# Performance work log

Hardware: AMD Instinct MI355X
Metric: run time of the kernel (lower is better)

## Reference

```python
import jax, jax.numpy as jnp
import numpy as np

N, E, C, D, H = 50000, 1600000, 50000, 128, 512


def setup_inputs() -> dict:
    key = jax.random.key(0)
    ks = jax.random.split(key, 16)
    s = jnp.float32(0.02)  # keep activations stable through 3 layers
    inp = {}
    inp["x"] = jax.random.normal(ks[0], (N, D), jnp.float32)
    inp["edge_index"] = jax.random.randint(ks[1], (2, E), 0, N)
    inp["first_edge"] = jax.random.randint(ks[2], (2,), 0, N)
    inp["candidate_edges"] = jax.random.randint(ks[3], (C, 2), 0, N)
    inp["t"] = jax.random.uniform(ks[4], (1, 1), jnp.float32)
    dims = [(D, H), (H, H), (H, H)]
    i = 5
    for l, (di, do) in enumerate(dims):
        inp[f"gin{l}_w1"] = jax.random.normal(ks[i], (di, do), jnp.float32) * s; i += 1
        inp[f"gin{l}_b1"] = jnp.zeros((do,), jnp.float32)
        inp[f"gin{l}_w2"] = jax.random.normal(ks[i], (do, do), jnp.float32) * s; i += 1
        inp[f"gin{l}_b2"] = jnp.zeros((do,), jnp.float32)
    inp["pred_w1"] = jax.random.normal(ks[i], (5 * H, H), jnp.float32) * s; i += 1
    inp["pred_b1"] = jnp.zeros((H,), jnp.float32)
    inp["pred_w2"] = jax.random.normal(ks[i], (H, 1), jnp.float32) * s; i += 1
    inp["pred_b2"] = jnp.zeros((1,), jnp.float32)
    inp["time_w1"] = jax.random.normal(ks[i], (1, H), jnp.float32) * s; i += 1
    inp["time_b1"] = jnp.zeros((H,), jnp.float32)
    inp["time_w2"] = jax.random.normal(ks[i], (H, H), jnp.float32) * s; i += 1
    inp["time_b2"] = jnp.zeros((H,), jnp.float32)
    return inp


def _edge_rep(x, u, v):
    # 'sum_absdiff': cat([x_u + x_v, |x_u - x_v|]) -> 2*H features
    xu, xv = x[u], x[v]
    return jnp.concatenate([xu + xv, jnp.abs(xu - xv)], axis=-1)


def reference(x, edge_index, first_edge, candidate_edges, t,
              gin0_w1, gin0_b1, gin0_w2, gin0_b2,
              gin1_w1, gin1_b1, gin1_w2, gin1_b2,
              gin2_w1, gin2_b1, gin2_w2, gin2_b2,
              pred_w1, pred_b1, pred_w2, pred_b2,
              time_w1, time_b1, time_w2, time_b2):
    src, dst = edge_index[0], edge_index[1]
    layers = [(gin0_w1, gin0_b1, gin0_w2, gin0_b2),
              (gin1_w1, gin1_b1, gin1_w2, gin1_b2),
              (gin2_w1, gin2_b1, gin2_w2, gin2_b2)]
    # GINConv (eps=0): h_i = MLP(x_i + sum_{j->i} x_j)
    for w1, b1, w2, b2 in layers:
        agg = jax.ops.segment_sum(x[src], dst, num_segments=x.shape[0])
        h = x + agg
        x = jax.nn.relu(h @ w1 + b1) @ w2 + b2
    first_feat = _edge_rep(x, first_edge[0], first_edge[1])  # [2H]
    t_embed = (jax.nn.relu(t @ time_w1 + time_b1) @ time_w2 + time_b2)[0]  # [H]
    cand_feat = _edge_rep(x, candidate_edges[:, 0], candidate_edges[:, 1])  # [C, 2H]
    Cn = cand_feat.shape[0]
    feat = jnp.concatenate([
        jnp.broadcast_to(first_feat, (Cn, first_feat.shape[0])),
        cand_feat,
        jnp.broadcast_to(t_embed, (Cn, t_embed.shape[0])),
    ], axis=-1)  # [C, 5H]
    logits = (jax.nn.relu(feat @ pred_w1 + pred_b1) @ pred_w2 + pred_b2)[:, 0]  # [C]
    return logits
```

## Files before the change

kernel.cpp:

```cpp
#include <hip/hip_runtime.h>

typedef __bf16 bf16x2 __attribute__((ext_vector_type(2)));
typedef __bf16 bf16x4 __attribute__((ext_vector_type(4)));
typedef __bf16 bf16x8 __attribute__((ext_vector_type(8)));
typedef float f32x4 __attribute__((ext_vector_type(4)));

#define CSR_CHUNKS 256

__device__ __forceinline__ void gload16(const __bf16* g, __bf16* l) {
    __builtin_amdgcn_global_load_lds((const __attribute__((address_space(1))) void*)g,
                                     (__attribute__((address_space(3))) void*)l, 16, 0, 0);
}

__global__ __launch_bounds__(256)
void hist_part_kernel(const int* __restrict__ dst, int* __restrict__ deg, int E, int N) {
    const int r = blockIdx.x & 7;
    const int chunk = blockIdx.x >> 3;
    const int RS = (N + 7) >> 3;
    const int lo = r * RS;
    const int hi = min(lo + RS, N);
    const int stride = CSR_CHUNKS * 256;
    for (int i = chunk * 256 + threadIdx.x; i < E; i += stride) {
        int d = dst[i];
        if (d >= lo && d < hi) atomicAdd(&deg[d], 1);
    }
}

__global__ __launch_bounds__(256)
void scatter_part_kernel(const int* __restrict__ src, const int* __restrict__ dst,
                         int* __restrict__ cursor, int* __restrict__ colsrc, int E, int N) {
    const int r = blockIdx.x & 7;
    const int chunk = blockIdx.x >> 3;
    const int RS = (N + 7) >> 3;
    const int lo = r * RS;
    const int hi = min(lo + RS, N);
    const int stride = CSR_CHUNKS * 256;
    for (int i = chunk * 256 + threadIdx.x; i < E; i += stride) {
        int d = dst[i];
        if (d >= lo && d < hi) {
            int p = atomicAdd(&cursor[d], 1);
            colsrc[p] = src[i];
        }
    }
}

__global__ __launch_bounds__(256)
void blocksum_kernel(const int* __restrict__ deg, int* __restrict__ bsum, int n) {
    __shared__ int red[256];
    int i = blockIdx.x * 256 + threadIdx.x;
    red[threadIdx.x] = (i < n) ? deg[i] : 0;
    __syncthreads();
    for (int off = 128; off > 0; off >>= 1) {
        if (threadIdx.x < off) red[threadIdx.x] += red[threadIdx.x + off];
        __syncthreads();
    }
    if (threadIdx.x == 0) bsum[blockIdx.x] = red[0];
}

__global__ __launch_bounds__(256)
void scanb_kernel(int* __restrict__ bsum, int nb) {
    __shared__ int s[256];
    int t = threadIdx.x;
    s[t] = (t < nb) ? bsum[t] : 0;
    __syncthreads();
    for (int off = 1; off < 256; off <<= 1) {
        int v = (t >= off) ? s[t - off] : 0;
        __syncthreads();
        s[t] += v;
        __syncthreads();
    }
    if (t < nb) bsum[t] = (t == 0) ? 0 : s[t - 1];
}

__global__ __launch_bounds__(256)
void scanw_kernel(const int* __restrict__ deg, const int* __restrict__ bsum,
                  int* __restrict__ rowptr, int* __restrict__ cursor, int n) {
    __shared__ int s[256];
    int b = blockIdx.x, t = threadIdx.x;
    int i = b * 256 + t;
    int d = (i < n) ? deg[i] : 0;
    s[t] = d;
    __syncthreads();
    for (int off = 1; off < 256; off <<= 1) {
        int v = (t >= off) ? s[t - off] : 0;
        __syncthreads();
        s[t] += v;
        __syncthreads();
    }
    int incl = s[t];
    int base = bsum[b];
    if (i < n) {
        int r = base + incl - d;
        rowptr[i] = r;
        cursor[i] = r;
        if (i == n - 1) rowptr[n] = base + incl;
    }
}

__global__ void f32_to_bf16_kernel(const float* __restrict__ in, __bf16* __restrict__ out, int n4) {
    int i = blockIdx.x * 256 + threadIdx.x;
    if (i < n4) {
        float4 f = ((const float4*)in)[i];
        bf16x4 o;
        o[0] = (__bf16)f.x; o[1] = (__bf16)f.y; o[2] = (__bf16)f.z; o[3] = (__bf16)f.w;
        ((bf16x4*)out)[i] = o;
    }
}

__global__ void wprep_kernel(const float* __restrict__ in, __bf16* __restrict__ out, int kbits) {
    int idx = blockIdx.x * 256 + threadIdx.x;
    int K = 1 << kbits;
    if (idx < (512 << kbits)) {
        int k = idx & (K - 1);
        int n = idx >> kbits;
        out[idx] = (__bf16)in[k * 512 + n];
    }
}

template<int F> struct VecT;
template<> struct VecT<2> { using T = bf16x2; };
template<> struct VecT<4> { using T = bf16x4; };
template<> struct VecT<8> { using T = bf16x8; };

template<int F, int U, int STR>
__global__ __launch_bounds__(256)
void agg_kernel(const __bf16* __restrict__ xb, const int* __restrict__ rowptr,
                const int* __restrict__ colsrc, __bf16* __restrict__ h, int n, int colbase) {
    const int node = blockIdx.x * 4 + (threadIdx.x >> 6);
    if (node >= n) return;
    const int lane = threadIdx.x & 63;
    using V = typename VecT<F>::T;

    const __bf16* xl = xb + colbase + lane * F;

    float acc[F];
    {
        V v = *(const V*)(xl + (size_t)node * STR);
        #pragma unroll
        for (int i = 0; i < F; i++) acc[i] = (float)v[i];
    }

    int e   = __builtin_amdgcn_readfirstlane(rowptr[node]);
    int end = __builtin_amdgcn_readfirstlane(rowptr[node + 1]);

    for (; e + U <= end; e += U) {
        int s[U];
        #pragma unroll
        for (int j = 0; j < U; j++) s[j] = colsrc[e + j];
        V v[U];
        #pragma unroll
        for (int j = 0; j < U; j++) v[j] = *(const V*)(xl + (size_t)s[j] * STR);
        #pragma unroll
        for (int j = 0; j < U; j++)
            #pragma unroll
            for (int i = 0; i < F; i++) acc[i] += (float)v[j][i];
    }
    if constexpr (U > 4) {
        for (; e + 4 <= end; e += 4) {
            int s[4];
            #pragma unroll
            for (int j = 0; j < 4; j++) s[j] = colsrc[e + j];
            V v[4];
            #pragma unroll
            for (int j = 0; j < 4; j++) v[j] = *(const V*)(xl + (size_t)s[j] * STR);
            #pragma unroll
            for (int j = 0; j < 4; j++)
                #pragma unroll
                for (int i = 0; i < F; i++) acc[i] += (float)v[j][i];
        }
    }
    for (; e < end; e++) {
        int s0 = colsrc[e];
        V v = *(const V*)(xl + (size_t)s0 * STR);
        #pragma unroll
        for (int i = 0; i < F; i++) acc[i] += (float)v[i];
    }

    __bf16* out = h + colbase + (size_t)node * STR + lane * F;
    V o;
    #pragma unroll
    for (int i = 0; i < F; i++) o[i] = (__bf16)acc[i];
    *(V*)out = o;
}

template<int AMODE, bool RELU>
__global__ __launch_bounds__(256, 3)
void gemm_kernel(const __bf16* __restrict__ A, const __bf16* __restrict__ Xb,
                 const int* __restrict__ cand, const __bf16* __restrict__ Bt,
                 const float* __restrict__ bias, __bf16* __restrict__ Cout,
                 int M, int K) {
    __shared__ __bf16 smem[2 * (2048 + 8192)];
    __bf16* const sA0 = smem;
    __bf16* const sA1 = smem + 2048;
    __bf16* const sB0 = smem + 4096;
    __bf16* const sB1 = smem + 4096 + 8192;

    const int tid = threadIdx.x;
    const int lane = tid & 63;
    const int wid = tid >> 6;
    const int mlane = lane & 15;
    const int quad = lane >> 4;
    const int rowBase = blockIdx.x * 64;
    const int nBase = blockIdx.y * 256;

    const int swzc = (((lane & 3) ^ ((lane >> 3) & 3)) << 3);

    const int aRow = rowBase + wid * 16 + (lane >> 2);
    const __bf16* aSrc = A + (size_t)aRow * K + swzc;
    const int bRow = nBase + wid * 64 + (lane >> 2);
    const __bf16* bSrc = Bt + (size_t)bRow * K + swzc;

    const int rkey = (mlane >> 1) & 3;
    const int base_r = mlane * 32 + ((quad ^ rkey) << 3);

    const int ar = tid >> 2;
    const int acn = tid & 3;
    const int ac = acn << 3;
    const int wkey = (ar >> 1) & 3;
    const int woffA = ar * 32 + ((acn ^ wkey) << 3);

    const f32x4 fzero = {0.f, 0.f, 0.f, 0.f};
    f32x4 acc[4][4];
    #pragma unroll
    for (int i = 0; i < 4; i++)
        #pragma unroll
        for (int j = 0; j < 4; j++) acc[i][j] = fzero;

    int uu = 0, vv = 0;
    const int grow = rowBase + ar;
    const bool arowok = (grow < M);
    if (AMODE == 1 && arowok) { uu = cand[2 * grow]; vv = cand[2 * grow + 1]; }

    bf16x8 pxu{}, pxv{};
    int pk = 0;

    auto stageB = [&](__bf16* bufB, int k0) {
        #pragma unroll
        for (int j = 0; j < 4; j++)
            gload16(bSrc + (size_t)j * 16 * K + k0, bufB + wid * 2048 + j * 512);
    };
    auto stageA0 = [&](__bf16* bufA, int k0) {
        if (aRow < M) gload16(aSrc + k0, bufA + wid * 512);
    };
    auto issueA1 = [&](int k0) {
        pk = k0;
        if (arowok) {
            int kk = (k0 + ac) & 511;
            pxu = *(const bf16x8*)(Xb + (size_t)uu * 512 + kk);
            pxv = *(const bf16x8*)(Xb + (size_t)vv * 512 + kk);
        }
    };
    auto commitA1 = [&](__bf16* bufA) {
        bf16x8 av = bf16x8{};
        if (arowok) {
            if (pk + ac < 512) {
                #pragma unroll
                for (int q = 0; q < 8; q++) av[q] = (__bf16)((float)pxu[q] + (float)pxv[q]);
            } else {
                #pragma unroll
                for (int q = 0; q < 8; q++) av[q] = (__bf16)fabsf((float)pxu[q] - (float)pxv[q]);
            }
        }
        *(bf16x8*)(bufA + woffA) = av;
    };

    auto compute = [&](const __bf16* bufA, const __bf16* bufB) {
        bf16x8 aF[4], bF[4];
        #pragma unroll
        for (int mt = 0; mt < 4; mt++)
            aF[mt] = *(const bf16x8*)(bufA + mt * 512 + base_r);
        #pragma unroll
        for (int nt = 0; nt < 4; nt++)
            bF[nt] = *(const bf16x8*)(bufB + wid * 2048 + nt * 512 + base_r);
        #pragma unroll
        for (int mt = 0; mt < 4; mt++)
            #pragma unroll
            for (int nt = 0; nt < 4; nt++)
                acc[mt][nt] = __builtin_amdgcn_mfma_f32_16x16x32_bf16(aF[mt], bF[nt], acc[mt][nt], 0, 0, 0);
    };

    const int nt = K >> 5;
    if (AMODE == 0) {
        stageA0(sA0, 0);
        stageB(sB0, 0);
        __syncthreads();
        for (int t = 0; t < nt; t += 2) {
            stageA0(sA1, (t + 1) << 5);
            stageB(sB1, (t + 1) << 5);
            compute(sA0, sB0);
            __syncthreads();
            if (t + 2 < nt) {
                stageA0(sA0, (t + 2) << 5);
                stageB(sB0, (t + 2) << 5);
            }
            compute(sA1, sB1);
            __syncthreads();
        }
    } else {
        issueA1(0);
        commitA1(sA0);
        stageB(sB0, 0);
        __syncthreads();
        for (int t = 0; t < nt; t += 2) {
            issueA1((t + 1) << 5);
            stageB(sB1, (t + 1) << 5);
            compute(sA0, sB0);
            commitA1(sA1);
            __syncthreads();
            if (t + 2 < nt) {
                issueA1((t + 2) << 5);
                stageB(sB0, (t + 2) << 5);
            }
            compute(sA1, sB1);
            if (t + 2 < nt) commitA1(sA0);
            __syncthreads();
        }
    }

    float bv[4];
    #pragma unroll
    for (int nt2 = 0; nt2 < 4; nt2++) bv[nt2] = bias[nBase + wid * 64 + nt2 * 16 + mlane];

    float* tp = (float*)smem;
    const int erow = tid >> 4;
    const int ecg = tid & 15;
    #pragma unroll
    for (int mt = 0; mt < 4; mt++) {
        __syncthreads();
        #pragma unroll
        for (int nt2 = 0; nt2 < 4; nt2++) {
            #pragma unroll
            for (int r = 0; r < 4; r++) {
                float v = acc[mt][nt2][r] + bv[nt2];
                if (RELU) v = fmaxf(v, 0.f);
                tp[(quad * 4 + r) * 260 + wid * 64 + nt2 * 16 + mlane] = v;
            }
        }
        __syncthreads();
        int gr = rowBase + mt * 16 + erow;
        if (gr < M) {
            const float* rp = tp + erow * 260 + ecg * 16;
            f32x4 a = *(const f32x4*)(rp);
            f32x4 b = *(const f32x4*)(rp + 4);
            f32x4 c = *(const f32x4*)(rp + 8);
            f32x4 d = *(const f32x4*)(rp + 12);
            bf16x8 o0, o1;
            #pragma unroll
            for (int j = 0; j < 4; j++) { o0[j] = (__bf16)a[j]; o0[4 + j] = (__bf16)b[j]; }
            #pragma unroll
            for (int j = 0; j < 4; j++) { o1[j] = (__bf16)c[j]; o1[4 + j] = (__bf16)d[j]; }
            __bf16* op = Cout + (size_t)gr * 512 + nBase + ecg * 16;
            *(bf16x8*)op = o0;
            *(bf16x8*)(op + 8) = o1;
        }
    }
}

__global__ __launch_bounds__(512)
void constvec_kernel(const __bf16* __restrict__ xb, const int* __restrict__ first_edge,
                     const float* __restrict__ t,
                     const float* __restrict__ tw1, const float* __restrict__ tb1,
                     const float* __restrict__ tw2, const float* __restrict__ tb2,
                     const float* __restrict__ pw1, const float* __restrict__ pb1,
                     float* __restrict__ cvec) {
    __shared__ float z1[512];
    __shared__ float te[512];
    __shared__ float ff[1024];
    int tid = threadIdx.x;
    float tv = t[0];
    z1[tid] = fmaxf(tv * tw1[tid] + tb1[tid], 0.f);
    int u = first_edge[0], v = first_edge[1];
    float xu = (float)xb[(size_t)u * 512 + tid];
    float xv = (float)xb[(size_t)v * 512 + tid];
    ff[tid] = xu + xv;
    ff[512 + tid] = fabsf(xu - xv);
    __syncthreads();
    float s = tb2[tid];
    for (int j = 0; j < 512; j++) s += z1[j] * tw2[j * 512 + tid];
    te[tid] = s;
    __syncthreads();
    float c = pb1[tid];
    for (int k = 0; k < 1024; k++) c += ff[k] * pw1[k * 512 + tid];
    for (int j = 0; j < 512; j++) c += te[j] * pw1[(2048 + j) * 512 + tid];
    cvec[tid] = c;
}

__global__ __launch_bounds__(256)
void logits_kernel(const __bf16* __restrict__ Z, const float* __restrict__ w2,
                   const float* __restrict__ b2, float* __restrict__ out, int C) {
    int c = blockIdx.x * 4 + (threadIdx.x >> 6);
    if (c >= C) return;
    int lane = threadIdx.x & 63;
    bf16x8 z = *(const bf16x8*)(Z + (size_t)c * 512 + lane * 8);
    const float4* w = (const float4*)(w2 + lane * 8);
    float4 w0 = w[0], w1 = w[1];
    float s = (float)z[0] * w0.x + (float)z[1] * w0.y + (float)z[2] * w0.z + (float)z[3] * w0.w
            + (float)z[4] * w1.x + (float)z[5] * w1.y + (float)z[6] * w1.z + (float)z[7] * w1.w;
    #pragma unroll
    for (int off = 32; off > 0; off >>= 1) s += __shfl_down(s, off);
    if (lane == 0) out[c] = s + b2[0];
}

extern "C" void kernel_launch(void* const* d_in, const int* in_sizes, int n_in,
                              void* d_out, int out_size, void* d_ws, size_t ws_size,
                              hipStream_t stream) {
    (void)n_in; (void)out_size; (void)ws_size;
    const float* x          = (const float*)d_in[0];
    const int*   edge_index = (const int*)d_in[1];
    const int*   first_edge = (const int*)d_in[2];
    const int*   cand       = (const int*)d_in[3];
    const float* t          = (const float*)d_in[4];
    const float* gw1[3] = {(const float*)d_in[5], (const float*)d_in[9],  (const float*)d_in[13]};
    const float* gb1[3] = {(const float*)d_in[6], (const float*)d_in[10], (const float*)d_in[14]};
    const float* gw2[3] = {(const float*)d_in[7], (const float*)d_in[11], (const float*)d_in[15]};
    const float* gb2[3] = {(const float*)d_in[8], (const float*)d_in[12], (const float*)d_in[16]};
    const float* pw1 = (const float*)d_in[17];
    const float* pb1 = (const float*)d_in[18];
    const float* pw2 = (const float*)d_in[19];
    const float* pb2 = (const float*)d_in[20];
    const float* tw1 = (const float*)d_in[21];
    const float* tb1 = (const float*)d_in[22];
    const float* tw2 = (const float*)d_in[23];
    const float* tb2 = (const float*)d_in[24];

    const int N = in_sizes[0] / 128;
    const int E = in_sizes[1] / 2;
    const int C = in_sizes[3] / 2;

    char* p = (char*)d_ws;
    auto alloc = [&](size_t bytes) -> void* {
        void* r = (void*)p;
        p += (bytes + 255) & ~(size_t)255;
        return r;
    };
    __bf16* h    = (__bf16*)alloc((size_t)N * 512 * 2);
    __bf16* u    = (__bf16*)alloc((size_t)N * 512 * 2);
    __bf16* xb   = (__bf16*)alloc((size_t)N * 512 * 2);
    __bf16* wt01 = (__bf16*)alloc((size_t)512 * 128 * 2);
    __bf16* wt02 = (__bf16*)alloc((size_t)512 * 512 * 2);
    __bf16* wt11 = (__bf16*)alloc((size_t)512 * 512 * 2);
    __bf16* wt12 = (__bf16*)alloc((size_t)512 * 512 * 2);
    __bf16* wt21 = (__bf16*)alloc((size_t)512 * 512 * 2);
    __bf16* wt22 = (__bf16*)alloc((size_t)512 * 512 * 2);
    __bf16* wtH  = (__bf16*)alloc((size_t)512 * 1024 * 2);
    int* rowptr = (int*)alloc((size_t)(N + 1) * 4);
    int* deg    = (int*)alloc((size_t)N * 4);
    int* cursor = (int*)alloc((size_t)N * 4);
    int* colsrc = (int*)alloc((size_t)E * 4);
    int* bsum   = (int*)alloc((size_t)256 * 4);
    float* cvec = (float*)alloc(512 * 4);
    __bf16* xb0 = (__bf16*)u;

    const int* src = edge_index;
    const int* dst = edge_index + E;

    hipMemsetAsync(deg, 0, (size_t)N * 4, stream);
    int nb = (N + 255) / 256;
    hist_part_kernel<<<CSR_CHUNKS * 8, 256, 0, stream>>>(dst, deg, E, N);
    blocksum_kernel<<<nb, 256, 0, stream>>>(deg, bsum, N);
    scanb_kernel<<<1, 256, 0, stream>>>(bsum, nb);
    scanw_kernel<<<nb, 256, 0, stream>>>(deg, bsum, rowptr, cursor, N);
    scatter_part_kernel<<<CSR_CHUNKS * 8, 256, 0, stream>>>(src, dst, cursor, colsrc, E, N);

    f32_to_bf16_kernel<<<((N * 128 / 4) + 255) / 256, 256, 0, stream>>>(x, xb0, N * 128 / 4);
    wprep_kernel<<<((512 << 7)  + 255) / 256, 256, 0, stream>>>(gw1[0], wt01, 7);
    wprep_kernel<<<((512 << 9)  + 255) / 256, 256, 0, stream>>>(gw2[0], wt02, 9);
    wprep_kernel<<<((512 << 9)  + 255) / 256, 256, 0, stream>>>(gw1[1], wt11, 9);
    wprep_kernel<<<((512 << 9)  + 255) / 256, 256, 0, stream>>>(gw2[1], wt12, 9);
    wprep_kernel<<<((512 << 9)  + 255) / 256, 256, 0, stream>>>(gw1[2], wt21, 9);
    wprep_kernel<<<((512 << 9)  + 255) / 256, 256, 0, stream>>>(gw2[2], wt22, 9);
    wprep_kernel<<<((512 << 10) + 255) / 256, 256, 0, stream>>>(pw1 + (size_t)1024 * 512, wtH, 10);

    dim3 ggrid((N + 63) / 64, 2);
    int ablocks = (N + 3) / 4;

    agg_kernel<2, 16, 128><<<ablocks, 256, 0, stream>>>(xb0, rowptr, colsrc, h, N, 0);
    gemm_kernel<0, true ><<<ggrid, 256, 0, stream>>>(h, nullptr, nullptr, wt01, gb1[0], u,  N, 128);
    gemm_kernel<0, false><<<ggrid, 256, 0, stream>>>(u, nullptr, nullptr, wt02, gb2[0], xb, N, 512);
    agg_kernel<4, 8, 512><<<ablocks, 256, 0, stream>>>(xb, rowptr, colsrc, h, N, 0);
    agg_kernel<4, 8, 512><<<ablocks, 256, 0, stream>>>(xb, rowptr, colsrc, h, N, 256);
    gemm_kernel<0, true ><<<ggrid, 256, 0, stream>>>(h, nullptr, nullptr, wt11, gb1[1], u,  N, 512);
    gemm_kernel<0, false><<<ggrid, 256, 0, stream>>>(u, nullptr, nullptr, wt12, gb2[1], xb, N, 512);
    agg_kernel<4, 8, 512><<<ablocks, 256, 0, stream>>>(xb, rowptr, colsrc, h, N, 0);
    agg_kernel<4, 8, 512><<<ablocks, 256, 0, stream>>>(xb, rowptr, colsrc, h, N, 256);
    gemm_kernel<0, true ><<<ggrid, 256, 0, stream>>>(h, nullptr, nullptr, wt21, gb1[2], u,  N, 512);
    gemm_kernel<0, false><<<ggrid, 256, 0, stream>>>(u, nullptr, nullptr, wt22, gb2[2], xb, N, 512);

    constvec_kernel<<<1, 512, 0, stream>>>(xb, first_edge, t, tw1, tb1, tw2, tb2, pw1, pb1, cvec);
    dim3 hgrid((C + 63) / 64, 2);
    gemm_kernel<1, true><<<hgrid, 256, 0, stream>>>(nullptr, xb, cand, wtH, cvec, u, C, 1024);
    logits_kernel<<<(C + 3) / 4, 256, 0, stream>>>(u, pw2, pb2, (float*)d_out, C);
}
```

Before: 1.202 ms.

## Keep two tile loads in flight with explicit vmcnt waits in GEMM loop

Restructures the AMODE==0 GEMM main loop so the next k-tile's global-to-LDS loads stay in flight while the current tile computes. Explicit s_waitcnt vmcnt(5) partial waits, raw s_barrier and sched_barrier calls replace the full __syncthreads drains. Out-of-range A rows are clamped to row M-1 so every thread issues a fixed number of loads, which keeps the vmcnt counting exact. The cost is reliance on precise counter accounting, and clamped rows load duplicate data that must not be stored.

```diff
diff --git a/kernel.cpp b/kernel.cpp
--- a/kernel.cpp
+++ b/kernel.cpp
@@ -206,7 +206,8 @@
     const int swzc = (((lane & 3) ^ ((lane >> 3) & 3)) << 3);
 
     const int aRow = rowBase + wid * 16 + (lane >> 2);
-    const __bf16* aSrc = A + (size_t)aRow * K + swzc;
+    const int aRowC = (aRow < M) ? aRow : (M - 1);
+    const __bf16* aSrc = A + (size_t)aRowC * K + swzc;
     const int bRow = nBase + wid * 64 + (lane >> 2);
     const __bf16* bSrc = Bt + (size_t)bRow * K + swzc;
 
@@ -240,7 +241,7 @@
             gload16(bSrc + (size_t)j * 16 * K + k0, bufB + wid * 2048 + j * 512);
     };
     auto stageA0 = [&](__bf16* bufA, int k0) {
-        if (aRow < M) gload16(aSrc + k0, bufA + wid * 512);
+        gload16(aSrc + k0, bufA + wid * 512);
     };
     auto issueA1 = [&](int k0) {
         pk = k0;
@@ -283,18 +284,32 @@
     if (AMODE == 0) {
         stageA0(sA0, 0);
         stageB(sB0, 0);
-        __syncthreads();
-        for (int t = 0; t < nt; t += 2) {
-            stageA0(sA1, (t + 1) << 5);
-            stageB(sB1, (t + 1) << 5);
-            compute(sA0, sB0);
-            __syncthreads();
-            if (t + 2 < nt) {
-                stageA0(sA0, (t + 2) << 5);
-                stageB(sB0, (t + 2) << 5);
+        __builtin_amdgcn_sched_barrier(0);
+        stageA0(sA1, 32);
+        stageB(sB1, 32);
+        asm volatile("s_waitcnt vmcnt(5)" ::: "memory");
+        __builtin_amdgcn_s_barrier();
+        __builtin_amdgcn_sched_barrier(0);
+
+        int cur = 0;
+        for (int t = 0; t < nt; ++t) {
+            __bf16* cA = cur ? sA1 : sA0;
+            __bf16* cB = cur ? sB1 : sB0;
+            compute(cA, cB);
+            if (t + 1 < nt) {
+                __builtin_amdgcn_s_barrier();
+                __builtin_amdgcn_sched_barrier(0);
+                if (t + 2 < nt) {
+                    stageA0(cA, (t + 2) << 5);
+                    stageB(cB, (t + 2) << 5);
+                    asm volatile("s_waitcnt vmcnt(5)" ::: "memory");
+                } else {
+                    asm volatile("s_waitcnt vmcnt(0)" ::: "memory");
+                }
+                __builtin_amdgcn_s_barrier();
+                __builtin_amdgcn_sched_barrier(0);
+                cur ^= 1;
             }
-            compute(sA1, sB1);
-            __syncthreads();
         }
     } else {
         issueA1(0);
```

Measured after the change: 1.201 ms. No clear change (-0.1%).

## Add 8-wave 128x256-tile GEMM with interleaved load/MFMA schedule for GIN layers

Applied to the files above, without the earlier changes.

Adds a new 512-thread GEMM kernel that computes a 128x256 output tile per block, with waves arranged 2x4 and a K-step of 64 split into four phases. Each phase interleaves LDS fragment reads, async global-to-LDS prefetch of the next tile, explicit barriers, waitcnts and setprio around MFMA bursts. It replaces the 256-thread 64x256 GEMM for all six GIN MLP matmuls, and the old kernel keeps only its candidate-gather mode. The aim is more data reuse per block and better overlap of memory with compute. In exchange it runs one block per CU with large LDS use, and clamping out-of-range A rows to M-1 means redundant loads on the tail tile.

```diff
diff --git a/kernel.cpp b/kernel.cpp
--- a/kernel.cpp
+++ b/kernel.cpp
@@ -183,6 +183,177 @@
     *(V*)out = o;
 }
 
+#define LDv(p) (*(const bf16x8*)(p))
+#define MM8(NTP) \
+  { acc[0][2*(NTP)]   = __builtin_amdgcn_mfma_f32_16x16x32_bf16(aF[0], bF0, acc[0][2*(NTP)],   0,0,0); \
+    acc[1][2*(NTP)]   = __builtin_amdgcn_mfma_f32_16x16x32_bf16(aF[1], bF0, acc[1][2*(NTP)],   0,0,0); \
+    acc[2][2*(NTP)]   = __builtin_amdgcn_mfma_f32_16x16x32_bf16(aF[2], bF0, acc[2][2*(NTP)],   0,0,0); \
+    acc[3][2*(NTP)]   = __builtin_amdgcn_mfma_f32_16x16x32_bf16(aF[3], bF0, acc[3][2*(NTP)],   0,0,0); \
+    acc[0][2*(NTP)+1] = __builtin_amdgcn_mfma_f32_16x16x32_bf16(aF[0], bF1, acc[0][2*(NTP)+1], 0,0,0); \
+    acc[1][2*(NTP)+1] = __builtin_amdgcn_mfma_f32_16x16x32_bf16(aF[1], bF1, acc[1][2*(NTP)+1], 0,0,0); \
+    acc[2][2*(NTP)+1] = __builtin_amdgcn_mfma_f32_16x16x32_bf16(aF[2], bF1, acc[2][2*(NTP)+1], 0,0,0); \
+    acc[3][2*(NTP)+1] = __builtin_amdgcn_mfma_f32_16x16x32_bf16(aF[3], bF1, acc[3][2*(NTP)+1], 0,0,0); }
+
+template<bool RELU>
+__global__ __launch_bounds__(512, 1)
+void gemm8_kernel(const __bf16* __restrict__ A, const __bf16* __restrict__ Bt,
+                  const float* __restrict__ bias, __bf16* __restrict__ Cout,
+                  int M, int K) {
+    __shared__ __bf16 smem[49152];
+    __bf16* const sA0 = smem;
+    __bf16* const sA1 = smem + 8192;
+    __bf16* const sB0 = smem + 16384;
+    __bf16* const sB1 = smem + 32768;
+
+    const int tid = threadIdx.x;
+    const int lane = tid & 63;
+    const int w = tid >> 6;
+    const int wr = w >> 2;
+    const int wc = w & 3;
+    const int mlane = lane & 15;
+    const int quad = lane >> 4;
+    const int rowBase = blockIdx.x * 128;
+    const int nBase = blockIdx.y * 256;
+
+    const int swz = (((lane & 3) ^ ((lane >> 3) & 3)) << 3);
+    int aR = rowBase + w * 16 + (lane >> 2);
+    if (aR >= M) aR = M - 1;
+    const __bf16* aSrc = A + (size_t)aR * K + swz;
+    const int bR0 = nBase + w * 16 + (lane >> 2);
+    const __bf16* bSrc = Bt + (size_t)bR0 * K + swz;
+
+    const int rkey = (mlane >> 1) & 3;
+    const int aRdBase = wr * 2048 + mlane * 32 + ((quad ^ rkey) << 3);
+    const int bRdBase = wc * 2048 + mlane * 32 + ((quad ^ rkey) << 3);
+
+    f32x4 acc[4][4];
+    #pragma unroll
+    for (int i = 0; i < 4; i++)
+        #pragma unroll
+        for (int j = 0; j < 4; j++) acc[i][j] = f32x4{0.f, 0.f, 0.f, 0.f};
+
+    auto stA = [&](__bf16* nbuf, int k0, int kk) {
+        gload16(aSrc + k0 + kk * 32, nbuf + kk * 4096 + w * 512);
+    };
+    auto stB = [&](__bf16* nbuf, int k0, int kk, int h) {
+        gload16(bSrc + (size_t)(h * 128) * K + k0 + kk * 32,
+                nbuf + kk * 8192 + h * 4096 + w * 512);
+    };
+
+    bf16x8 aF[4], bF0, bF1;
+
+    stA(sA0, 0, 0); stB(sB0, 0, 0, 0); stB(sB0, 0, 0, 1);
+    stA(sA0, 0, 1); stB(sB0, 0, 1, 0); stB(sB0, 0, 1, 1);
+    asm volatile("s_waitcnt vmcnt(3)" ::: "memory");
+    __builtin_amdgcn_sched_barrier(0);
+    __builtin_amdgcn_s_barrier();
+
+    const int NT = K >> 6;
+    for (int t = 0; t < NT; ++t) {
+        __bf16* const cA = (t & 1) ? sA1 : sA0;
+        __bf16* const cB = (t & 1) ? sB1 : sB0;
+        __bf16* const nA = (t & 1) ? sA0 : sA1;
+        __bf16* const nB = (t & 1) ? sB0 : sB1;
+        const int kn = (t + 1) << 6;
+        const bool more = (t + 1 < NT);
+
+        aF[0] = LDv(cA + aRdBase);
+        aF[1] = LDv(cA + 512 + aRdBase);
+        aF[2] = LDv(cA + 1024 + aRdBase);
+        aF[3] = LDv(cA + 1536 + aRdBase);
+        bF0 = LDv(cB + bRdBase);
+        bF1 = LDv(cB + 512 + bRdBase);
+        if (more) { stA(nA, kn, 0); stB(nB, kn, 0, 0); }
+        __builtin_amdgcn_s_barrier();
+        asm volatile("s_waitcnt lgkmcnt(0)" ::: "memory");
+        __builtin_amdgcn_sched_barrier(0);
+        __builtin_amdgcn_s_setprio(1);
+        MM8(0);
+        __builtin_amdgcn_s_setprio(0);
+        __builtin_amdgcn_s_barrier();
+
+        bF0 = LDv(cB + 1024 + bRdBase);
+        bF1 = LDv(cB + 1536 + bRdBase);
+        if (more) stB(nB, kn, 0, 1);
+        __builtin_amdgcn_s_barrier();
+        asm volatile("s_waitcnt lgkmcnt(0)" ::: "memory");
+        __builtin_amdgcn_sched_barrier(0);
+        __builtin_amdgcn_s_setprio(1);
+        MM8(1);
+        __builtin_amdgcn_s_setprio(0);
+        if (more) { asm volatile("s_waitcnt vmcnt(3)" ::: "memory"); }
+        else      { asm volatile("s_waitcnt vmcnt(0)" ::: "memory"); }
+        __builtin_amdgcn_sched_barrier(0);
+        __builtin_amdgcn_s_barrier();
+
+        aF[0] = LDv(cA + 4096 + aRdBase);
+        aF[1] = LDv(cA + 4096 + 512 + aRdBase);
+        aF[2] = LDv(cA + 4096 + 1024 + aRdBase);
+        aF[3] = LDv(cA + 4096 + 1536 + aRdBase);
+        bF0 = LDv(cB + 8192 + bRdBase);
+        bF1 = LDv(cB + 8192 + 512 + bRdBase);
+        if (more) { stA(nA, kn, 1); stB(nB, kn, 1, 0); }
+        __builtin_amdgcn_s_barrier();
+        asm volatile("s_waitcnt lgkmcnt(0)" ::: "memory");
+        __builtin_amdgcn_sched_barrier(0);
+        __builtin_amdgcn_s_setprio(1);
+        MM8(0);
+        __builtin_amdgcn_s_setprio(0);
+        __builtin_amdgcn_s_barrier();
+
+        bF0 = LDv(cB + 8192 + 1024 + bRdBase);
+        bF1 = LDv(cB + 8192 + 1536 + bRdBase);
+        if (more) stB(nB, kn, 1, 1);
+        __builtin_amdgcn_s_barrier();
+        asm volatile("s_waitcnt lgkmcnt(0)" ::: "memory");
+        __builtin_amdgcn_sched_barrier(0);
+        __builtin_amdgcn_s_setprio(1);
+        MM8(1);
+        __builtin_amdgcn_s_setprio(0);
+        if (more) { asm volatile("s_waitcnt vmcnt(3)" ::: "memory"); }
+        __builtin_amdgcn_sched_barrier(0);
+        __builtin_amdgcn_s_barrier();
+    }
+
+    float bv[4];
+    #pragma unroll
+    for (int nt = 0; nt < 4; nt++) bv[nt] = bias[nBase + wc * 64 + nt * 16 + mlane];
+
+    float* tp = (float*)smem;
+    const int srow = tid >> 4;
+    const int scg = tid & 15;
+    #pragma unroll
+    for (int mt = 0; mt < 4; mt++) {
+        __syncthreads();
+        #pragma unroll
+        for (int nt = 0; nt < 4; nt++) {
+            #pragma unroll
+            for (int r = 0; r < 4; r++) {
+                float v = acc[mt][nt][r] + bv[nt];
+                if (RELU) v = fmaxf(v, 0.f);
+                tp[(wr * 16 + quad * 4 + r) * 260 + wc * 64 + nt * 16 + mlane] = v;
+            }
+        }
+        __syncthreads();
+        int gr = rowBase + (srow >> 4) * 64 + mt * 16 + (srow & 15);
+        if (gr < M) {
+            const float* rp = tp + srow * 260 + scg * 16;
+            f32x4 a = *(const f32x4*)(rp);
+            f32x4 b = *(const f32x4*)(rp + 4);
+            f32x4 c = *(const f32x4*)(rp + 8);
+            f32x4 d = *(const f32x4*)(rp + 12);
+            bf16x8 o0, o1;
+            #pragma unroll
+            for (int j = 0; j < 4; j++) { o0[j] = (__bf16)a[j]; o0[4 + j] = (__bf16)b[j]; }
+            #pragma unroll
+            for (int j = 0; j < 4; j++) { o1[j] = (__bf16)c[j]; o1[4 + j] = (__bf16)d[j]; }
+            __bf16* op = Cout + (size_t)gr * 512 + nBase + scg * 16;
+            *(bf16x8*)op = o0;
+            *(bf16x8*)(op + 8) = o1;
+        }
+    }
+}
+
 template<int AMODE, bool RELU>
 __global__ __launch_bounds__(256, 3)
 void gemm_kernel(const __bf16* __restrict__ A, const __bf16* __restrict__ Xb,
@@ -204,9 +375,6 @@
     const int nBase = blockIdx.y * 256;
 
     const int swzc = (((lane & 3) ^ ((lane >> 3) & 3)) << 3);
-
-    const int aRow = rowBase + wid * 16 + (lane >> 2);
-    const __bf16* aSrc = A + (size_t)aRow * K + swzc;
     const int bRow = nBase + wid * 64 + (lane >> 2);
     const __bf16* bSrc = Bt + (size_t)bRow * K + swzc;
 
@@ -219,12 +387,11 @@
     const int wkey = (ar >> 1) & 3;
     const int woffA = ar * 32 + ((acn ^ wkey) << 3);
 
-    const f32x4 fzero = {0.f, 0.f, 0.f, 0.f};
     f32x4 acc[4][4];
     #pragma unroll
     for (int i = 0; i < 4; i++)
         #pragma unroll
-        for (int j = 0; j < 4; j++) acc[i][j] = fzero;
+        for (int j = 0; j < 4; j++) acc[i][j] = f32x4{0.f, 0.f, 0.f, 0.f};
 
     int uu = 0, vv = 0;
     const int grow = rowBase + ar;
@@ -238,9 +405,6 @@
         #pragma unroll
         for (int j = 0; j < 4; j++)
             gload16(bSrc + (size_t)j * 16 * K + k0, bufB + wid * 2048 + j * 512);
-    };
-    auto stageA0 = [&](__bf16* bufA, int k0) {
-        if (aRow < M) gload16(aSrc + k0, bufA + wid * 512);
     };
     auto issueA1 = [&](int k0) {
         pk = k0;
@@ -280,41 +444,23 @@
     };
 
     const int nt = K >> 5;
-    if (AMODE == 0) {
-        stageA0(sA0, 0);
-        stageB(sB0, 0);
-        __syncthreads();
-        for (int t = 0; t < nt; t += 2) {
-            stageA0(sA1, (t + 1) << 5);
-            stageB(sB1, (t + 1) << 5);
-            compute(sA0, sB0);
-            __syncthreads();
-            if (t + 2 < nt) {
-                stageA0(sA0, (t + 2) << 5);
-                stageB(sB0, (t + 2) << 5);
-            }
-            compute(sA1, sB1);
-            __syncthreads();
-        }
-    } else {
-        issueA1(0);
-        commitA1(sA0);
-        stageB(sB0, 0);
-        __syncthreads();
-        for (int t = 0; t < nt; t += 2) {
-            issueA1((t + 1) << 5);
-            stageB(sB1, (t + 1) << 5);
-            compute(sA0, sB0);
-            commitA1(sA1);
-            __syncthreads();
-            if (t + 2 < nt) {
-                issueA1((t + 2) << 5);
-                stageB(sB0, (t + 2) << 5);
-            }
-            compute(sA1, sB1);
-            if (t + 2 < nt) commitA1(sA0);
-            __syncthreads();
-        }
+    issueA1(0);
+    commitA1(sA0);
+    stageB(sB0, 0);
+    __syncthreads();
+    for (int t = 0; t < nt; t += 2) {
+        issueA1((t + 1) << 5);
+        stageB(sB1, (t + 1) << 5);
+        compute(sA0, sB0);
+        commitA1(sA1);
+        __syncthreads();
+        if (t + 2 < nt) {
+            issueA1((t + 2) << 5);
+            stageB(sB0, (t + 2) << 5);
+        }
+        compute(sA1, sB1);
+        if (t + 2 < nt) commitA1(sA0);
+        __syncthreads();
     }
 
     float bv[4];
@@ -471,20 +617,20 @@
     wprep_kernel<<<((512 << 9)  + 255) / 256, 256, 0, stream>>>(gw2[2], wt22, 9);
     wprep_kernel<<<((512 << 10) + 255) / 256, 256, 0, stream>>>(pw1 + (size_t)1024 * 512, wtH, 10);
 
-    dim3 ggrid((N + 63) / 64, 2);
+    dim3 g8((N + 127) / 128, 2);
     int ablocks = (N + 3) / 4;
 
     agg_kernel<2, 16, 128><<<ablocks, 256, 0, stream>>>(xb0, rowptr, colsrc, h, N, 0);
-    gemm_kernel<0, true ><<<ggrid, 256, 0, stream>>>(h, nullptr, nullptr, wt01, gb1[0], u,  N, 128);
-    gemm_kernel<0, false><<<ggrid, 256, 0, stream>>>(u, nullptr, nullptr, wt02, gb2[0], xb, N, 512);
+    gemm8_kernel<true ><<<g8, 512, 0, stream>>>(h, wt01, gb1[0], u,  N, 128);
+    gemm8_kernel<false><<<g8, 512, 0, stream>>>(u, wt02, gb2[0], xb, N, 512);
     agg_kernel<4, 8, 512><<<ablocks, 256, 0, stream>>>(xb, rowptr, colsrc, h, N, 0);
     agg_kernel<4, 8, 512><<<ablocks, 256, 0, stream>>>(xb, rowptr, colsrc, h, N, 256);
-    gemm_kernel<0, true ><<<ggrid, 256, 0, stream>>>(h, nullptr, nullptr, wt11, gb1[1], u,  N, 512);
-    gemm_kernel<0, false><<<ggrid, 256, 0, stream>>>(u, nullptr, nullptr, wt12, gb2[1], xb, N, 512);
+    gemm8_kernel<true ><<<g8, 512, 0, stream>>>(h, wt11, gb1[1], u,  N, 512);
+    gemm8_kernel<false><<<g8, 512, 0, stream>>>(u, wt12, gb2[1], xb, N, 512);
     agg_kernel<4, 8, 512><<<ablocks, 256, 0, stream>>>(xb, rowptr, colsrc, h, N, 0);
     agg_kernel<4, 8, 512><<<ablocks, 256, 0, stream>>>(xb, rowptr, colsrc, h, N, 256);
-    gemm_kernel<0, true ><<<ggrid, 256, 0, stream>>>(h, nullptr, nullptr, wt21, gb1[2], u,  N, 512);
-    gemm_kernel<0, false><<<ggrid, 256, 0, stream>>>(u, nullptr, nullptr, wt22, gb2[2], xb, N, 512);
+    gemm8_kernel<true ><<<g8, 512, 0, stream>>>(h, wt21, gb1[2], u,  N, 512);
+    gemm8_kernel<false><<<g8, 512, 0, stream>>>(u, wt22, gb2[2], xb, N, 512);
 
     constvec_kernel<<<1, 512, 0, stream>>>(xb, first_edge, t, tw1, tb1, tw2, tb2, pw1, pb1, cvec);
     dim3 hgrid((C + 63) / 64, 2);
```

Result: slower. 1.261 ms (+5.0%).
